# Performance work log

Hardware: AMD Instinct MI355X
Metric: run time of the kernel (lower is better)

The kernel has to match this reference:

```python
import jax, jax.numpy as jnp
import numpy as np
from jax import lax

NUM_FILTERS = 180
DN = ('NCHW', 'OIHW', 'NCHW')


def _gabor_kernel(freq, theta, sigma_x, sigma_y, n_stds=3):
    # real part of skimage.filters.gabor_kernel
    ct, st = np.cos(theta), np.sin(theta)
    x0 = int(np.ceil(max(abs(n_stds * sigma_x * ct), abs(n_stds * sigma_y * st), 1)))
    y0 = int(np.ceil(max(abs(n_stds * sigma_y * ct), abs(n_stds * sigma_x * st), 1)))
    y, x = np.mgrid[-y0:y0 + 1, -x0:x0 + 1]
    rotx = x * ct + y * st
    roty = -x * st + y * ct
    g = np.exp(-0.5 * (rotx ** 2 / sigma_x ** 2 + roty ** 2 / sigma_y ** 2))
    g /= 2.0 * np.pi * sigma_x * sigma_y
    return g * np.cos(2.0 * np.pi * freq * rotx)  # Re{exp(1j*2*pi*f*rotx)}


def _make_weights(sigma_x, sigma_y, freq, num_filters):
    kernels = [
        _gabor_kernel(freq, theta=np.pi - th, sigma_x=sigma_x, sigma_y=sigma_y)
        for th in np.linspace(0, np.pi * (num_filters - 1) / num_filters, num_filters)
    ]
    s = max(max(k.shape) for k in kernels)  # 17 for defaults
    kernels = np.stack([
        np.pad(k, [[(s - k.shape[0]) // 2], [(s - k.shape[1]) // 2]]) for k in kernels
    ])
    return kernels.astype(np.float32)


def _gauss1d(sigma, truncate=4.0):
    # matches scipy.ndimage gaussian kernel (skimage default truncate=4.0)
    r = int(truncate * sigma + 0.5)
    xs = np.arange(-r, r + 1, dtype=np.float64)
    k = np.exp(-0.5 * (xs / sigma) ** 2)
    return (k / k.sum()).astype(np.float32), r


def _gaussian_blur(img, sigma):
    # separable blur with edge-replicate ('nearest') padding, img: [B,1,H,W]
    k, r = _gauss1d(sigma)
    kh = jnp.asarray(k).reshape(1, 1, -1, 1)
    kw = jnp.asarray(k).reshape(1, 1, 1, -1)
    p = jnp.pad(img, ((0, 0), (0, 0), (r, r), (0, 0)), mode='edge')
    img = lax.conv_general_dilated(p, kh, (1, 1), 'VALID', dimension_numbers=DN)
    p = jnp.pad(img, ((0, 0), (0, 0), (0, 0), (r, r)), mode='edge')
    return lax.conv_general_dilated(p, kw, (1, 1), 'VALID', dimension_numbers=DN)


def setup_inputs() -> dict:
    key = jax.random.key(0)
    x = jax.random.uniform(key, (2, 3, 512, 512), dtype=jnp.float32)
    weights = jnp.asarray(_make_weights(1.8, 2.4, 0.23, NUM_FILTERS))[:, None, :, :]  # [180,1,17,17]
    bins = jnp.asarray(
        np.linspace(0, np.pi * (NUM_FILTERS - 1) / NUM_FILTERS, NUM_FILTERS), jnp.float32
    ).reshape(1, -1, 1, 1)
    return {'x': x, 'weights': weights, 'bins': bins}


def reference(x, weights, bins):
    # rgb -> gray, [B,1,H,W]
    gray = (0.2989 * x[:, 0] + 0.587 * x[:, 1] + 0.114 * x[:, 2])[:, None]
    # difference of gaussians (skimage, low=0.4, high=10.0)
    filtered = _gaussian_blur(gray, 0.4) - _gaussian_blur(gray, 10.0)
    kh, kw = weights.shape[2], weights.shape[3]
    response = lax.conv_general_dilated(
        filtered, weights, (1, 1), ((kh // 2, kh // 2), (kw // 2, kw // 2)),
        dimension_numbers=DN)  # [B,180,H,W]
    response = jnp.abs(response)
    idx = jnp.argmax(response, axis=1)[:, None]  # [B,1,H,W]
    orientation_map = idx.astype(jnp.float32) / NUM_FILTERS * 255.0
    orientation_map_rad = orientation_map / NUM_FILTERS * jnp.pi
    d0 = jnp.abs(orientation_map_rad - bins)
    dists = jnp.minimum(d0, jnp.minimum(jnp.abs(orientation_map_rad - bins - jnp.pi),
                                        jnp.abs(orientation_map_rad - bins + jnp.pi)))
    F_orients_norm = response / jnp.sum(response, axis=1, keepdims=True)
    confidence_map = jnp.sum(dists ** 2 * F_orients_norm, axis=1)  # [B,H,W]
    return orientation_map, confidence_map
```

## Files before the change

### kernel.cpp

```cpp
#include <hip/hip_runtime.h>
#include <math.h>
#include <stdint.h>

#define H 512
#define W 512
#define NPIX (H * W)
#define NB 2
#define NF 180
#define KS 17
#define WSCALE 1024.0f

#define RAW_OFF 0
#define HP_OFF  1440
#define LP_OFF  2880
#define POOL_U32 4320
#define BCH_U32 3072

typedef _Float16 half8 __attribute__((ext_vector_type(8)));
typedef float floatx16 __attribute__((ext_vector_type(16)));
typedef uint32_t u32x4 __attribute__((ext_vector_type(4)));

union FragU { u32x4 u; half8 h; };

__global__ void k_taps(float* __restrict__ taps) {
  if (threadIdx.x == 0 && blockIdx.x == 0) {
    {
      double k[5], s = 0.0;
      for (int i = 0; i < 5; i++) { double xv = (double)(i - 2) / 0.4; k[i] = exp(-0.5 * xv * xv); s += k[i]; }
      for (int i = 0; i < 5; i++) taps[i] = (float)(k[i] / s);
    }
    {
      double k[81], s = 0.0;
      for (int i = 0; i < 81; i++) { double xv = (double)(i - 40) / 10.0; k[i] = exp(-0.5 * xv * xv); s += k[i]; }
      for (int i = 0; i < 81; i++) taps[8 + i] = (float)(k[i] / s);
    }
  }
}

__global__ void k_repackB(const float* __restrict__ w, uint32_t* __restrict__ Bf) {
  int tid = blockIdx.x * 256 + threadIdx.x;
  if (tid >= 19 * 6 * 64 * 4) return;
  int q = tid & 3;
  int lane = (tid >> 2) & 63;
  int ct = tid >> 8;
  int t = ct % 6, c = ct / 6;
  int n = t * 32 + (lane & 31);
  int hf = lane >> 5;
  uint32_t hv = 0, lv = 0;
  for (int s = 0; s < 2; s++) {
    int j = 2 * q + s;
    int k = hf * 8 + j;
    float val = 0.f;
    if (n < NF) {
      if (c < 17)       val = w[n * 289 + c * 17 + k];
      else if (c == 17) val = w[n * 289 + k * 17 + 16];
      else if (k == 0)  val = w[n * 289 + 16 * 17 + 16];
    }
    val *= WSCALE;
    _Float16 hh = (_Float16)val;
    _Float16 ll = (_Float16)(val - (float)hh);
    hv |= (uint32_t)__builtin_bit_cast(uint16_t, hh) << (16 * s);
    lv |= (uint32_t)__builtin_bit_cast(uint16_t, ll) << (16 * s);
  }
  int base = c * 3072;
  int off = t * 256 + lane * 4 + q;
  Bf[base + off] = hv;
  Bf[base + 1536 + off] = lv;
}

__global__ void k_gray(const float* __restrict__ x, float* __restrict__ gray) {
  int i = blockIdx.x * blockDim.x + threadIdx.x;
  if (i >= NB * NPIX) return;
  int b = i / NPIX, r = i % NPIX;
  const float* xb = x + (size_t)b * 3 * NPIX;
  gray[i] = 0.2989f * xb[r] + 0.587f * xb[NPIX + r] + 0.114f * xb[2 * NPIX + r];
}

__global__ void k_vblur2(const float* __restrict__ in, float* __restrict__ outA,
                         float* __restrict__ outB, const float* __restrict__ taps) {
  int i = blockIdx.x * blockDim.x + threadIdx.x;
  if (i >= NB * NPIX) return;
  int b = i / NPIX, r = i % NPIX;
  int y = r / W, xx = r % W;
  const float* img = in + (size_t)b * NPIX;
  float a = 0.f;
#pragma unroll
  for (int j = -2; j <= 2; j++) {
    int yy = y + j; yy = yy < 0 ? 0 : (yy > H - 1 ? H - 1 : yy);
    a = fmaf(taps[j + 2], img[yy * W + xx], a);
  }
  float c = 0.f;
  for (int j = -40; j <= 40; j++) {
    int yy = y + j; yy = yy < 0 ? 0 : (yy > H - 1 ? H - 1 : yy);
    c = fmaf(taps[8 + j + 40], img[yy * W + xx], c);
  }
  outA[i] = a;
  outB[i] = c;
}

__global__ void k_hblur_dog(const float* __restrict__ inA, const float* __restrict__ inB,
                            uint32_t* __restrict__ dogp, const float* __restrict__ taps) {
  int i = blockIdx.x * blockDim.x + threadIdx.x;
  if (i >= NB * NPIX) return;
  int b = i / NPIX, r = i % NPIX;
  int y = r / W, xx = r % W;
  const float* ra = inA + (size_t)b * NPIX + (size_t)y * W;
  const float* rb = inB + (size_t)b * NPIX + (size_t)y * W;
  float a = 0.f;
#pragma unroll
  for (int j = -2; j <= 2; j++) {
    int xc = xx + j; xc = xc < 0 ? 0 : (xc > W - 1 ? W - 1 : xc);
    a = fmaf(taps[j + 2], ra[xc], a);
  }
  float c = 0.f;
  for (int j = -40; j <= 40; j++) {
    int xc = xx + j; xc = xc < 0 ? 0 : (xc > W - 1 ? W - 1 : xc);
    c = fmaf(taps[8 + j + 40], rb[xc], c);
  }
  float d = a - c;
  _Float16 hh = (_Float16)d;
  _Float16 ll = (_Float16)(d - (float)hh);
  dogp[i] = ((uint32_t)__builtin_bit_cast(uint16_t, ll) << 16) |
            (uint32_t)__builtin_bit_cast(uint16_t, hh);
}

__launch_bounds__(256, 2)
__global__ void k_conv(const uint32_t* __restrict__ dogp,
                       const uint32_t* __restrict__ Bf,
                       const float* __restrict__ bins,
                       float* __restrict__ out) {
  __shared__ uint32_t pool[POOL_U32];

  const int b  = blockIdx.z;
  const int y0 = blockIdx.y * 2;
  const int x0 = blockIdx.x * 64;
  const int tid = threadIdx.x;
  const int lane = tid & 63;
  const int w  = __builtin_amdgcn_readfirstlane(tid >> 6);
  const int fg  = w & 1;
  const int ch  = w >> 1;
  const int nl = lane & 31;
  const int half = lane >> 5;

  const uint32_t* dgb = dogp + (size_t)b * NPIX;
  for (int i = tid; i < 18 * 80; i += 256) {
    int ry = i / 80, rx = i % 80;
    int gy = y0 + ry - 8, gx = x0 + rx - 8;
    uint32_t v = 0;
    if (gy >= 0 && gy < H && gx >= 0 && gx < W) v = dgb[gy * W + gx];
    pool[RAW_OFF + i] = v;
  }
  __syncthreads();
  for (int i = tid; i < 18 * 80; i += 256) {
    int c = i % 80;
    uint32_t v0 = pool[RAW_OFF + i];
    uint32_t v1 = (c < 79) ? pool[RAW_OFF + i + 1] : 0u;
    pool[HP_OFF + i] = __builtin_amdgcn_perm(v1, v0, 0x05040100u);
    pool[LP_OFF + i] = __builtin_amdgcn_perm(v1, v0, 0x07060302u);
  }
  __syncthreads();

  floatx16 acc[2][3];
#pragma unroll
  for (int d = 0; d < 2; d++)
#pragma unroll
    for (int t = 0; t < 3; t++)
#pragma unroll
      for (int q = 0; q < 16; q++) acc[d][t][q] = 0.f;

  const int abase = ch * 32 + nl + half * 8;

  auto buildRow = [&](int tr, FragU& fh, FragU& fl) {
    const uint32_t* hp = &pool[HP_OFF + tr * 80 + abase];
    const uint32_t* lp = &pool[LP_OFF + tr * 80 + abase];
#pragma unroll
    for (int q = 0; q < 4; q++) {
      fh.u[q] = hp[2 * q];
      fl.u[q] = lp[2 * q];
    }
  };
  auto buildStrip = [&](int c, int rb, FragU& fh, FragU& fl) {
    int kyb = (c - 17) * 16 + half * 8;
    uint32_t d[8];
#pragma unroll
    for (int j = 0; j < 8; j++) {
      int ky = kyb + j; if (ky > 16) ky = 16;
      d[j] = pool[RAW_OFF + (rb + ky) * 80 + ch * 32 + nl + 16];
    }
#pragma unroll
    for (int q = 0; q < 4; q++) {
      fh.u[q] = __builtin_amdgcn_perm(d[2 * q + 1], d[2 * q], 0x05040100u);
      fl.u[q] = __builtin_amdgcn_perm(d[2 * q + 1], d[2 * q], 0x07060302u);
    }
  };
  auto mfma18 = [&](FragU* wh, FragU* wl,
                    FragU& d0h, FragU& d0l, FragU& d1h, FragU& d1l) {
#pragma unroll
    for (int t = 0; t < 3; t++) {
      acc[0][t] = __builtin_amdgcn_mfma_f32_32x32x16_f16(wh[t].h, d0h.h, acc[0][t], 0, 0, 0);
      acc[1][t] = __builtin_amdgcn_mfma_f32_32x32x16_f16(wh[t].h, d1h.h, acc[1][t], 0, 0, 0);
    }
#pragma unroll
    for (int t = 0; t < 3; t++) {
      acc[0][t] = __builtin_amdgcn_mfma_f32_32x32x16_f16(wh[t].h, d0l.h, acc[0][t], 0, 0, 0);
      acc[1][t] = __builtin_amdgcn_mfma_f32_32x32x16_f16(wh[t].h, d1l.h, acc[1][t], 0, 0, 0);
    }
#pragma unroll
    for (int t = 0; t < 3; t++) {
      acc[0][t] = __builtin_amdgcn_mfma_f32_32x32x16_f16(wl[t].h, d0h.h, acc[0][t], 0, 0, 0);
      acc[1][t] = __builtin_amdgcn_mfma_f32_32x32x16_f16(wl[t].h, d1h.h, acc[1][t], 0, 0, 0);
    }
  };

  const uint32_t* wbh = Bf + (size_t)(3 * fg) * 256 + (size_t)lane * 4;
  const uint32_t* wbl = wbh + 1536;

  FragU wch[3], wcl[3], wnh[3], wnl2[3];
#pragma unroll
  for (int t = 0; t < 3; t++) {
    wch[t].u = *(const u32x4*)(wbh + t * 256);
    wcl[t].u = *(const u32x4*)(wbl + t * 256);
  }

  FragU a0h, a0l, a1h, a1l;
  buildRow(0, a0h, a0l);

#pragma unroll
  for (int c = 0; c < 17; c++) {
    const uint32_t* nbh = wbh + (size_t)(c + 1) * BCH_U32;
    const uint32_t* nbl = wbl + (size_t)(c + 1) * BCH_U32;
#pragma unroll
    for (int t = 0; t < 3; t++) {
      wnh[t].u  = *(const u32x4*)(nbh + t * 256);
      wnl2[t].u = *(const u32x4*)(nbl + t * 256);
    }
    buildRow(c + 1, a1h, a1l);
    mfma18(wch, wcl, a0h, a0l, a1h, a1l);
    a0h = a1h; a0l = a1l;
#pragma unroll
    for (int t = 0; t < 3; t++) { wch[t] = wnh[t]; wcl[t] = wnl2[t]; }
  }
  {
    const uint32_t* nbh = wbh + (size_t)18 * BCH_U32;
    const uint32_t* nbl = wbl + (size_t)18 * BCH_U32;
#pragma unroll
    for (int t = 0; t < 3; t++) {
      wnh[t].u  = *(const u32x4*)(nbh + t * 256);
      wnl2[t].u = *(const u32x4*)(nbl + t * 256);
    }
    FragU s0h, s0l, s1h, s1l;
    buildStrip(17, 0, s0h, s0l);
    buildStrip(17, 1, s1h, s1l);
    mfma18(wch, wcl, s0h, s0l, s1h, s1l);
#pragma unroll
    for (int t = 0; t < 3; t++) { wch[t] = wnh[t]; wcl[t] = wnl2[t]; }
  }
  {
    FragU s0h, s0l, s1h, s1l;
    buildStrip(18, 0, s0h, s0l);
    buildStrip(18, 1, s1h, s1l);
    mfma18(wch, wcl, s0h, s0l, s1h, s1l);
  }
  __syncthreads();

  float* pm = (float*)&pool[0];
  int*   pn = (int*)&pool[256];
  float* pS = (float*)&pool[512];
  float* pc = (float*)&pool[768];
  int*   fn = (int*)&pool[1024];
  float* fS = (float*)&pool[1152];

  const float PI_F = 3.14159265358979323846f;
  const float INV_PI = 0.31830988618379067154f;
  const double STEPD = 3.14159265358979323846 * 179.0 / 180.0 / 179.0;
  const float stepf = (float)STEPD;
  const float hbase = (4.0f * (float)half) * stepf;
  const int colp = ch * 32 + nl;

#pragma unroll
  for (int d = 0; d < 2; d++) {
    float m = -1.f; int n = 0; float S0 = 0.f, S1 = 0.f;
#pragma unroll
    for (int t = 0; t < 3; t++) {
#pragma unroll
      for (int q = 0; q < 16; q++) {
        float v = fabsf(acc[d][t][q]);
        if (q & 1) S1 += v; else S0 += v;
        int nf = 32 * (3 * fg + t) + (q & 3) + 8 * (q >> 2) + 4 * half;
        if (v > m) { m = v; n = nf; }
      }
    }
    float S = S0 + S1;
    float mo = __shfl_xor(m, 32);
    int   no = __shfl_xor(n, 32);
    float So = __shfl_xor(S, 32);
    bool take = (mo > m) || (mo == m && no < n);
    if (take) { m = mo; n = no; }
    S += So;
    if (half == 0) {
      int o = (d * 2 + fg) * 64 + colp;
      pm[o] = m; pn[o] = n; pS[o] = S;
    }
  }
  __syncthreads();

  if (fg == 0) {
#pragma unroll
    for (int d = 0; d < 2; d++) {
      int o0 = (d * 2 + 0) * 64 + colp;
      int o1 = (d * 2 + 1) * 64 + colp;
      float m0 = pm[o0], m1 = pm[o1];
      int n = (m1 > m0) ? pn[o1] : pn[o0];
      float S = pS[o0] + pS[o1];
      float om = (float)n / 180.0f * 255.0f;
      if (half == 0) {
        fn[d * 64 + colp] = n; fS[d * 64 + colp] = S;
        out[(size_t)b * NPIX + (size_t)(y0 + d) * W + x0 + colp] = om;
      }
    }
  }
  __syncthreads();

#pragma unroll
  for (int d = 0; d < 2; d++) {
    int nwin = fn[d * 64 + colp];
    float om = (float)nwin / 180.0f * 255.0f;
    float rad = om / 180.0f * PI_F;
    float ddc = rad - hbase;
    float C0 = 0.f, C1 = 0.f;
#pragma unroll
    for (int t = 0; t < 3; t++) {
#pragma unroll
      for (int q = 0; q < 16; q++) {
        const float K = (float)((double)(32 * (3 * fg + t) + (q & 3) + 8 * (q >> 2)) * STEPD);
        float dd = ddc - K;
        float r = rintf(dd * INV_PI);
        float dist = fmaf(-PI_F, r, dd);
        float w2 = dist * dist;
        if (q & 1) C1 = fmaf(w2, fabsf(acc[d][t][q]), C1);
        else       C0 = fmaf(w2, fabsf(acc[d][t][q]), C0);
      }
    }
    float C = C0 + C1;
    C += __shfl_xor(C, 32);
    if (half == 0) pc[(d * 2 + fg) * 64 + colp] = C;
  }
  __syncthreads();

  if (fg == 0) {
#pragma unroll
    for (int d = 0; d < 2; d++) {
      float C = pc[(d * 2 + 0) * 64 + colp] + pc[(d * 2 + 1) * 64 + colp];
      if (half == 0) {
        out[(size_t)NB * NPIX + (size_t)b * NPIX + (size_t)(y0 + d) * W + x0 + colp]
            = C / fS[d * 64 + colp];
      }
    }
  }
}

extern "C" void kernel_launch(void* const* d_in, const int* in_sizes, int n_in,
                              void* d_out, int out_size, void* d_ws, size_t ws_size,
                              hipStream_t stream) {
  const float* x = (const float*)d_in[0];
  const float* wts = (const float*)d_in[1];
  const float* bins = (const float*)d_in[2];
  float* out = (float*)d_out;

  float* ws = (float*)d_ws;
  float* gray = ws;
  float* tmpA = ws + (size_t)NB * NPIX;
  float* tmpB = tmpA + (size_t)NB * NPIX;
  uint32_t* dogp = (uint32_t*)(tmpB + (size_t)NB * NPIX);
  float* taps = (float*)(dogp + (size_t)NB * NPIX);
  uint32_t* Bf = (uint32_t*)(taps + 128);

  k_taps<<<1, 64, 0, stream>>>(taps);
  k_repackB<<<114, 256, 0, stream>>>(wts, Bf);

  int n = NB * NPIX;
  int blk = 256, grd = (n + blk - 1) / blk;
  k_gray<<<grd, blk, 0, stream>>>(x, gray);
  k_vblur2<<<grd, blk, 0, stream>>>(gray, tmpA, tmpB, taps);
  k_hblur_dog<<<grd, blk, 0, stream>>>(tmpA, tmpB, dogp, taps);

  dim3 g(W / 64, H / 2, NB);
  k_conv<<<g, 256, 0, stream>>>(dogp, Bf, bins, out);
}
```

Measured before the change: 190.8 us.

## Vectorize preprocessing kernels and double-buffer conv weights with MFMA priority

The gray, vertical blur and horizontal blur/DoG kernels now each handle four pixels per thread with float4 loads and stores. The horizontal blur keeps an interior fast path that reuses a register window instead of doing per-tap clamped loads. In the conv kernel, the weight and row loop becomes a two-buffer ping-pong that drops the register copies, and the MFMA bursts get raised wave priority via s_setprio. These target memory-instruction overhead in the preprocessing stages and issue contention in the conv loop. The cost is higher register pressure, especially the 21-float4 window in hblur.

```diff
diff --git a/kernel.cpp b/kernel.cpp
--- a/kernel.cpp
+++ b/kernel.cpp
@@ -70,58 +70,103 @@
 
 __global__ void k_gray(const float* __restrict__ x, float* __restrict__ gray) {
   int i = blockIdx.x * blockDim.x + threadIdx.x;
-  if (i >= NB * NPIX) return;
-  int b = i / NPIX, r = i % NPIX;
+  if (i >= NB * NPIX / 4) return;
+  int b = i / (NPIX / 4), r4 = (i % (NPIX / 4)) * 4;
   const float* xb = x + (size_t)b * 3 * NPIX;
-  gray[i] = 0.2989f * xb[r] + 0.587f * xb[NPIX + r] + 0.114f * xb[2 * NPIX + r];
+  float4 rv = *(const float4*)&xb[r4];
+  float4 gv = *(const float4*)&xb[NPIX + r4];
+  float4 bv = *(const float4*)&xb[2 * NPIX + r4];
+  float4 o;
+  o.x = 0.2989f * rv.x + 0.587f * gv.x + 0.114f * bv.x;
+  o.y = 0.2989f * rv.y + 0.587f * gv.y + 0.114f * bv.y;
+  o.z = 0.2989f * rv.z + 0.587f * gv.z + 0.114f * bv.z;
+  o.w = 0.2989f * rv.w + 0.587f * gv.w + 0.114f * bv.w;
+  *(float4*)&gray[(size_t)b * NPIX + r4] = o;
 }
 
 __global__ void k_vblur2(const float* __restrict__ in, float* __restrict__ outA,
                          float* __restrict__ outB, const float* __restrict__ taps) {
   int i = blockIdx.x * blockDim.x + threadIdx.x;
-  if (i >= NB * NPIX) return;
-  int b = i / NPIX, r = i % NPIX;
-  int y = r / W, xx = r % W;
+  if (i >= NB * NPIX / 4) return;
+  int b = i / (NPIX / 4), r = i % (NPIX / 4);
+  int y = r / (W / 4), x4 = (r % (W / 4)) * 4;
   const float* img = in + (size_t)b * NPIX;
-  float a = 0.f;
+  float4 a = {0.f, 0.f, 0.f, 0.f};
 #pragma unroll
   for (int j = -2; j <= 2; j++) {
     int yy = y + j; yy = yy < 0 ? 0 : (yy > H - 1 ? H - 1 : yy);
-    a = fmaf(taps[j + 2], img[yy * W + xx], a);
-  }
-  float c = 0.f;
+    float4 v = *(const float4*)&img[yy * W + x4];
+    float t = taps[j + 2];
+    a.x = fmaf(t, v.x, a.x); a.y = fmaf(t, v.y, a.y);
+    a.z = fmaf(t, v.z, a.z); a.w = fmaf(t, v.w, a.w);
+  }
+  float4 c = {0.f, 0.f, 0.f, 0.f};
   for (int j = -40; j <= 40; j++) {
     int yy = y + j; yy = yy < 0 ? 0 : (yy > H - 1 ? H - 1 : yy);
-    c = fmaf(taps[8 + j + 40], img[yy * W + xx], c);
-  }
-  outA[i] = a;
-  outB[i] = c;
+    float4 v = *(const float4*)&img[yy * W + x4];
+    float t = taps[8 + j + 40];
+    c.x = fmaf(t, v.x, c.x); c.y = fmaf(t, v.y, c.y);
+    c.z = fmaf(t, v.z, c.z); c.w = fmaf(t, v.w, c.w);
+  }
+  *(float4*)&outA[(size_t)b * NPIX + y * W + x4] = a;
+  *(float4*)&outB[(size_t)b * NPIX + y * W + x4] = c;
 }
 
 __global__ void k_hblur_dog(const float* __restrict__ inA, const float* __restrict__ inB,
                             uint32_t* __restrict__ dogp, const float* __restrict__ taps) {
   int i = blockIdx.x * blockDim.x + threadIdx.x;
-  if (i >= NB * NPIX) return;
-  int b = i / NPIX, r = i % NPIX;
-  int y = r / W, xx = r % W;
+  if (i >= NB * NPIX / 4) return;
+  int b = i / (NPIX / 4), r = i % (NPIX / 4);
+  int y = r / (W / 4), x4 = (r % (W / 4)) * 4;
   const float* ra = inA + (size_t)b * NPIX + (size_t)y * W;
   const float* rb = inB + (size_t)b * NPIX + (size_t)y * W;
-  float a = 0.f;
-#pragma unroll
-  for (int j = -2; j <= 2; j++) {
-    int xc = xx + j; xc = xc < 0 ? 0 : (xc > W - 1 ? W - 1 : xc);
-    a = fmaf(taps[j + 2], ra[xc], a);
-  }
-  float c = 0.f;
-  for (int j = -40; j <= 40; j++) {
-    int xc = xx + j; xc = xc < 0 ? 0 : (xc > W - 1 ? W - 1 : xc);
-    c = fmaf(taps[8 + j + 40], rb[xc], c);
-  }
-  float d = a - c;
-  _Float16 hh = (_Float16)d;
-  _Float16 ll = (_Float16)(d - (float)hh);
-  dogp[i] = ((uint32_t)__builtin_bit_cast(uint16_t, ll) << 16) |
+  float res[4];
+  if (x4 >= 40 && x4 <= 468) {
+    float4 sa[3];
+#pragma unroll
+    for (int k = 0; k < 3; k++) sa[k] = *(const float4*)&ra[x4 - 4 + 4 * k];
+    float4 sb[21];
+#pragma unroll
+    for (int k = 0; k < 21; k++) sb[k] = *(const float4*)&rb[x4 - 40 + 4 * k];
+    const float* pa = (const float*)sa;
+    const float* pb = (const float*)sb;
+#pragma unroll
+    for (int p = 0; p < 4; p++) {
+      float a = 0.f;
+#pragma unroll
+      for (int j = -2; j <= 2; j++) a = fmaf(taps[j + 2], pa[p + j + 4], a);
+      float c = 0.f;
+      for (int j = -40; j <= 40; j++) c = fmaf(taps[8 + j + 40], pb[p + j + 40], c);
+      res[p] = a - c;
+    }
+  } else {
+#pragma unroll
+    for (int p = 0; p < 4; p++) {
+      int xx = x4 + p;
+      float a = 0.f;
+#pragma unroll
+      for (int j = -2; j <= 2; j++) {
+        int xc = xx + j; xc = xc < 0 ? 0 : (xc > W - 1 ? W - 1 : xc);
+        a = fmaf(taps[j + 2], ra[xc], a);
+      }
+      float c = 0.f;
+      for (int j = -40; j <= 40; j++) {
+        int xc = xx + j; xc = xc < 0 ? 0 : (xc > W - 1 ? W - 1 : xc);
+        c = fmaf(taps[8 + j + 40], rb[xc], c);
+      }
+      res[p] = a - c;
+    }
+  }
+  uint32_t pk[4];
+#pragma unroll
+  for (int p = 0; p < 4; p++) {
+    float d = res[p];
+    _Float16 hh = (_Float16)d;
+    _Float16 ll = (_Float16)(d - (float)hh);
+    pk[p] = ((uint32_t)__builtin_bit_cast(uint16_t, ll) << 16) |
             (uint32_t)__builtin_bit_cast(uint16_t, hh);
+  }
+  *(u32x4*)&dogp[(size_t)b * NPIX + (size_t)y * W + x4] = *(u32x4*)pk;
 }
 
 __launch_bounds__(256, 2)
@@ -193,8 +238,20 @@
       fl.u[q] = __builtin_amdgcn_perm(d[2 * q + 1], d[2 * q], 0x07060302u);
     }
   };
+  const uint32_t* wbh = Bf + (size_t)(3 * fg) * 256 + (size_t)lane * 4;
+  const uint32_t* wbl = wbh + 1536;
+  auto loadW = [&](int c, FragU* wh, FragU* wl) {
+    const uint32_t* bh = wbh + (size_t)c * BCH_U32;
+    const uint32_t* bl = wbl + (size_t)c * BCH_U32;
+#pragma unroll
+    for (int t = 0; t < 3; t++) {
+      wh[t].u = *(const u32x4*)(bh + t * 256);
+      wl[t].u = *(const u32x4*)(bl + t * 256);
+    }
+  };
   auto mfma18 = [&](FragU* wh, FragU* wl,
                     FragU& d0h, FragU& d0l, FragU& d1h, FragU& d1l) {
+    __builtin_amdgcn_s_setprio(1);
 #pragma unroll
     for (int t = 0; t < 3; t++) {
       acc[0][t] = __builtin_amdgcn_mfma_f32_32x32x16_f16(wh[t].h, d0h.h, acc[0][t], 0, 0, 0);
@@ -210,56 +267,38 @@
       acc[0][t] = __builtin_amdgcn_mfma_f32_32x32x16_f16(wl[t].h, d0h.h, acc[0][t], 0, 0, 0);
       acc[1][t] = __builtin_amdgcn_mfma_f32_32x32x16_f16(wl[t].h, d1h.h, acc[1][t], 0, 0, 0);
     }
+    __builtin_amdgcn_s_setprio(0);
   };
 
-  const uint32_t* wbh = Bf + (size_t)(3 * fg) * 256 + (size_t)lane * 4;
-  const uint32_t* wbl = wbh + 1536;
-
-  FragU wch[3], wcl[3], wnh[3], wnl2[3];
-#pragma unroll
-  for (int t = 0; t < 3; t++) {
-    wch[t].u = *(const u32x4*)(wbh + t * 256);
-    wcl[t].u = *(const u32x4*)(wbl + t * 256);
-  }
-
-  FragU a0h, a0l, a1h, a1l;
-  buildRow(0, a0h, a0l);
-
-#pragma unroll
-  for (int c = 0; c < 17; c++) {
-    const uint32_t* nbh = wbh + (size_t)(c + 1) * BCH_U32;
-    const uint32_t* nbl = wbl + (size_t)(c + 1) * BCH_U32;
-#pragma unroll
-    for (int t = 0; t < 3; t++) {
-      wnh[t].u  = *(const u32x4*)(nbh + t * 256);
-      wnl2[t].u = *(const u32x4*)(nbl + t * 256);
-    }
-    buildRow(c + 1, a1h, a1l);
-    mfma18(wch, wcl, a0h, a0l, a1h, a1l);
-    a0h = a1h; a0l = a1l;
-#pragma unroll
-    for (int t = 0; t < 3; t++) { wch[t] = wnh[t]; wcl[t] = wnl2[t]; }
-  }
+  FragU wAh[3], wAl[3], wBh[3], wBl[3];
+  loadW(0, wAh, wAl);
+  FragU aPh, aPl, aQh, aQl;
+  buildRow(0, aPh, aPl);
+
+#pragma unroll
+  for (int p = 0; p < 8; p++) {
+    loadW(2 * p + 1, wBh, wBl);
+    buildRow(2 * p + 1, aQh, aQl);
+    mfma18(wAh, wAl, aPh, aPl, aQh, aQl);
+    loadW(2 * p + 2, wAh, wAl);
+    buildRow(2 * p + 2, aPh, aPl);
+    mfma18(wBh, wBl, aQh, aQl, aPh, aPl);
+  }
+  loadW(17, wBh, wBl);
+  buildRow(17, aQh, aQl);
+  mfma18(wAh, wAl, aPh, aPl, aQh, aQl);
   {
-    const uint32_t* nbh = wbh + (size_t)18 * BCH_U32;
-    const uint32_t* nbl = wbl + (size_t)18 * BCH_U32;
-#pragma unroll
-    for (int t = 0; t < 3; t++) {
-      wnh[t].u  = *(const u32x4*)(nbh + t * 256);
-      wnl2[t].u = *(const u32x4*)(nbl + t * 256);
-    }
+    loadW(18, wAh, wAl);
     FragU s0h, s0l, s1h, s1l;
     buildStrip(17, 0, s0h, s0l);
     buildStrip(17, 1, s1h, s1l);
-    mfma18(wch, wcl, s0h, s0l, s1h, s1l);
-#pragma unroll
-    for (int t = 0; t < 3; t++) { wch[t] = wnh[t]; wcl[t] = wnl2[t]; }
+    mfma18(wBh, wBl, s0h, s0l, s1h, s1l);
   }
   {
     FragU s0h, s0l, s1h, s1l;
     buildStrip(18, 0, s0h, s0l);
     buildStrip(18, 1, s1h, s1l);
-    mfma18(wch, wcl, s0h, s0l, s1h, s1l);
+    mfma18(wAh, wAl, s0h, s0l, s1h, s1l);
   }
   __syncthreads();
 
@@ -378,11 +417,11 @@
   k_taps<<<1, 64, 0, stream>>>(taps);
   k_repackB<<<114, 256, 0, stream>>>(wts, Bf);
 
-  int n = NB * NPIX;
-  int blk = 256, grd = (n + blk - 1) / blk;
-  k_gray<<<grd, blk, 0, stream>>>(x, gray);
-  k_vblur2<<<grd, blk, 0, stream>>>(gray, tmpA, tmpB, taps);
-  k_hblur_dog<<<grd, blk, 0, stream>>>(tmpA, tmpB, dogp, taps);
+  int n4 = NB * NPIX / 4;
+  int blk = 256, grd4 = (n4 + blk - 1) / blk;
+  k_gray<<<grd4, blk, 0, stream>>>(x, gray);
+  k_vblur2<<<grd4, blk, 0, stream>>>(gray, tmpA, tmpB, taps);
+  k_hblur_dog<<<grd4, blk, 0, stream>>>(tmpA, tmpB, dogp, taps);
 
   dim3 g(W / 64, H / 2, NB);
   k_conv<<<g, 256, 0, stream>>>(dogp, Bf, bins, out);
```

New measurement: 206.1 us. 8.0% more time.
